# Performance work log

Hardware: AMD Instinct MI355X
Metric: run time of the kernel (lower is better)

## Reference

```python
import jax, jax.numpy as jnp
import numpy as np

B, S, D = 64, 2048, 64

def setup_inputs() -> dict:
    key = jax.random.key(0)
    kq, kk, kv = jax.random.split(key, 3)
    queries = jax.random.normal(kq, (B, S, D), dtype=jnp.float32)
    keys = jax.random.normal(kk, (B, S, D), dtype=jnp.float32)
    values = jax.random.normal(kv, (B, S, D), dtype=jnp.float32)
    return {"queries": queries, "keys": keys, "values": values}

def reference(queries, keys, values):
    # scores: [B, Sq, Sk] = Q @ K^T / sqrt(d)
    d = queries.shape[-1]
    scale = 1.0 / jnp.sqrt(jnp.asarray(d, dtype=queries.dtype))
    scores = jnp.einsum('bqd,bkd->bqk', queries, keys) * scale
    attn = jax.nn.softmax(scores, axis=-1)
    # dropout is identity in eval/reference mode
    return jnp.einsum('bqk,bkd->bqd', attn, values)
```

## Files before the change

kernel.cpp:

```cpp
#include <hip/hip_runtime.h>


typedef short bf16x8 __attribute__((ext_vector_type(8)));
typedef float f32x16 __attribute__((ext_vector_type(16)));

#define SQK 0.18033688011112042f

__device__ __forceinline__ short f2bf(float x) {
  unsigned u = __float_as_uint(x);
  u = (u + 0x7fffu + ((u >> 16) & 1u)) >> 16;
  return (short)u;
}

__device__ __forceinline__ unsigned pk2(float lo, float hi) {
  unsigned r;
  asm("v_cvt_pk_bf16_f32 %0, %1, %2" : "=v"(r) : "v"(lo), "v"(hi));
  return r;
}

#define SM_HALF(ZV, OFF, RS, PUV)                                        \
  {                                                                      \
    float e0 = __builtin_amdgcn_exp2f(ZV[OFF + 0]);                      \
    float e1 = __builtin_amdgcn_exp2f(ZV[OFF + 1]);                      \
    float e2 = __builtin_amdgcn_exp2f(ZV[OFF + 2]);                      \
    float e3 = __builtin_amdgcn_exp2f(ZV[OFF + 3]);                      \
    float e4 = __builtin_amdgcn_exp2f(ZV[OFF + 4]);                      \
    float e5 = __builtin_amdgcn_exp2f(ZV[OFF + 5]);                      \
    float e6 = __builtin_amdgcn_exp2f(ZV[OFF + 6]);                      \
    float e7 = __builtin_amdgcn_exp2f(ZV[OFF + 7]);                      \
    RS += ((e0 + e1) + (e2 + e3)) + ((e4 + e5) + (e6 + e7));             \
    union { bf16x8 v; unsigned u[4]; } pu_;                              \
    pu_.u[0] = pk2(e0, e1); pu_.u[1] = pk2(e2, e3);                      \
    pu_.u[2] = pk2(e4, e5); pu_.u[3] = pk2(e6, e7);                      \
    PUV = pu_.v;                                                         \
  }

__global__ __launch_bounds__(512, 2) void DotProductAttention_44573170598739_kernel(
    const float* __restrict__ Q, const float* __restrict__ K,
    const float* __restrict__ V, float* __restrict__ O) {
  constexpr int S = 2048, D = 64;
  const int b   = blockIdx.x;
  const int q0  = blockIdx.y * 512;
  const int tid = threadIdx.x;
  const int w    = tid >> 6;
  const int lane = tid & 63;
  const int hi   = lane >> 5;
  const int r32  = lane & 31;

  __shared__ __align__(16) short ksh[2][32 * 72];
  __shared__ __align__(16) short vsh[2][64 * 40];

  bf16x8 qf0[4], qf1[4];
#pragma unroll
  for (int dd = 0; dd < 4; ++dd) {
    const float* qp = Q + ((size_t)b * S + q0 + w * 64 + r32) * D + dd * 16 + hi * 8;
    float4 x = ((const float4*)qp)[0];
    float4 y = ((const float4*)qp)[1];
    bf16x8 f;
    f[0] = f2bf(x.x * SQK); f[1] = f2bf(x.y * SQK);
    f[2] = f2bf(x.z * SQK); f[3] = f2bf(x.w * SQK);
    f[4] = f2bf(y.x * SQK); f[5] = f2bf(y.y * SQK);
    f[6] = f2bf(y.z * SQK); f[7] = f2bf(y.w * SQK);
    qf0[dd] = f;
  }
#pragma unroll
  for (int dd = 0; dd < 4; ++dd) {
    const float* qp = Q + ((size_t)b * S + q0 + w * 64 + 32 + r32) * D + dd * 16 + hi * 8;
    float4 x = ((const float4*)qp)[0];
    float4 y = ((const float4*)qp)[1];
    bf16x8 f;
    f[0] = f2bf(x.x * SQK); f[1] = f2bf(x.y * SQK);
    f[2] = f2bf(x.z * SQK); f[3] = f2bf(x.w * SQK);
    f[4] = f2bf(y.x * SQK); f[5] = f2bf(y.y * SQK);
    f[6] = f2bf(y.z * SQK); f[7] = f2bf(y.w * SQK);
    qf1[dd] = f;
  }

  f32x16 oa00 = {}, oa01 = {}, oa10 = {}, oa11 = {};
  float rs0 = 0.f, rs1 = 0.f;
  const f32x16 z16c = {};

  const float* Kb = K + (size_t)b * S * D;
  const float* Vb = V + (size_t)b * S * D;

  const int vcb = 16 * (w >> 2) + (((w & 1) << 3) | ((w & 2) << 1));

  float4 kx;
  float  vv[4];

  kx = ((const float4*)Kb)[tid];
#pragma unroll
  for (int j = 0; j < 4; ++j)
    vv[j] = Vb[(w * 4 + j) * D + lane];
  {
    int f = 4 * tid;
    int row = f >> 6, col = f & 63;
    uint2 pk = { pk2(kx.x, kx.y), pk2(kx.z, kx.w) };
    *(uint2*)&ksh[0][row * 72 + col] = pk;
  }
  {
    uint2 pv = { pk2(vv[0], vv[1]), pk2(vv[2], vv[3]) };
    *(uint2*)&vsh[0][lane * 40 + vcb] = pv;
  }
  kx = ((const float4*)(Kb + 32 * D))[tid];
#pragma unroll
  for (int j = 0; j < 4; ++j)
    vv[j] = Vb[(32 + w * 4 + j) * D + lane];
  __syncthreads();

  int p = 0;
  for (int kt = 0; kt < S; kt += 32, p ^= 1) {
    if (kt + 32 < S) {
      {
        int f = 4 * tid;
        int row = f >> 6, col = f & 63;
        uint2 pk = { pk2(kx.x, kx.y), pk2(kx.z, kx.w) };
        *(uint2*)&ksh[p ^ 1][row * 72 + col] = pk;
      }
      {
        uint2 pv = { pk2(vv[0], vv[1]), pk2(vv[2], vv[3]) };
        *(uint2*)&vsh[p ^ 1][lane * 40 + vcb] = pv;
      }
      if (kt + 64 < S) {
        const float* Kg2 = Kb + (size_t)(kt + 64) * D;
        const float* Vg2 = Vb + (size_t)(kt + 64) * D;
        kx = ((const float4*)Kg2)[tid];
#pragma unroll
        for (int j = 0; j < 4; ++j)
          vv[j] = Vg2[(w * 4 + j) * D + lane];
      }
    }

    const short* kshp = ksh[p];
    const short* vshp = vsh[p];

    bf16x8 kf[4];
#pragma unroll
    for (int dd = 0; dd < 4; ++dd)
      kf[dd] = *(const bf16x8*)&kshp[r32 * 72 + dd * 16 + hi * 8];

    bf16x8 vf00 = *(const bf16x8*)&vshp[r32 * 40 + hi * 8];
    bf16x8 vf01 = *(const bf16x8*)&vshp[(32 + r32) * 40 + hi * 8];
    bf16x8 vf10 = *(const bf16x8*)&vshp[r32 * 40 + 16 + hi * 8];
    bf16x8 vf11 = *(const bf16x8*)&vshp[(32 + r32) * 40 + 16 + hi * 8];

    {
      __builtin_amdgcn_s_setprio(1);
      f32x16 z = __builtin_amdgcn_mfma_f32_32x32x16_bf16(kf[0], qf0[0], z16c, 0, 0, 0);
      z = __builtin_amdgcn_mfma_f32_32x32x16_bf16(kf[1], qf0[1], z, 0, 0, 0);
      z = __builtin_amdgcn_mfma_f32_32x32x16_bf16(kf[2], qf0[2], z, 0, 0, 0);
      z = __builtin_amdgcn_mfma_f32_32x32x16_bf16(kf[3], qf0[3], z, 0, 0, 0);
      __builtin_amdgcn_s_setprio(0);

      bf16x8 pa;
      SM_HALF(z, 0, rs0, pa);
      __builtin_amdgcn_s_setprio(1);
      oa00 = __builtin_amdgcn_mfma_f32_32x32x16_bf16(pa, vf00, oa00, 0, 0, 0);
      oa01 = __builtin_amdgcn_mfma_f32_32x32x16_bf16(pa, vf01, oa01, 0, 0, 0);
      __builtin_amdgcn_s_setprio(0);
      SM_HALF(z, 8, rs0, pa);
      __builtin_amdgcn_s_setprio(1);
      oa00 = __builtin_amdgcn_mfma_f32_32x32x16_bf16(pa, vf10, oa00, 0, 0, 0);
      oa01 = __builtin_amdgcn_mfma_f32_32x32x16_bf16(pa, vf11, oa01, 0, 0, 0);
      __builtin_amdgcn_s_setprio(0);
    }

    {
      __builtin_amdgcn_s_setprio(1);
      f32x16 z = __builtin_amdgcn_mfma_f32_32x32x16_bf16(kf[0], qf1[0], z16c, 0, 0, 0);
      z = __builtin_amdgcn_mfma_f32_32x32x16_bf16(kf[1], qf1[1], z, 0, 0, 0);
      z = __builtin_amdgcn_mfma_f32_32x32x16_bf16(kf[2], qf1[2], z, 0, 0, 0);
      z = __builtin_amdgcn_mfma_f32_32x32x16_bf16(kf[3], qf1[3], z, 0, 0, 0);
      __builtin_amdgcn_s_setprio(0);

      bf16x8 pa;
      SM_HALF(z, 0, rs1, pa);
      __builtin_amdgcn_s_setprio(1);
      oa10 = __builtin_amdgcn_mfma_f32_32x32x16_bf16(pa, vf00, oa10, 0, 0, 0);
      oa11 = __builtin_amdgcn_mfma_f32_32x32x16_bf16(pa, vf01, oa11, 0, 0, 0);
      __builtin_amdgcn_s_setprio(0);
      SM_HALF(z, 8, rs1, pa);
      __builtin_amdgcn_s_setprio(1);
      oa10 = __builtin_amdgcn_mfma_f32_32x32x16_bf16(pa, vf10, oa10, 0, 0, 0);
      oa11 = __builtin_amdgcn_mfma_f32_32x32x16_bf16(pa, vf11, oa11, 0, 0, 0);
      __builtin_amdgcn_s_setprio(0);
    }
    __syncthreads();
  }

  {
    float tot = rs0 + __shfl_xor(rs0, 32);
#pragma unroll
    for (int g = 0; g < 16; ++g) {
      int rq = (g & 3) + 8 * (g >> 2) + 4 * hi;
      float inv = 1.0f / __shfl(tot, rq);
      int q = q0 + w * 64 + rq;
      float* op = O + ((size_t)b * S + q) * D + r32;
      op[0]  = oa00[g] * inv;
      op[32] = oa01[g] * inv;
    }
  }
  {
    float tot = rs1 + __shfl_xor(rs1, 32);
#pragma unroll
    for (int g = 0; g < 16; ++g) {
      int rq = (g & 3) + 8 * (g >> 2) + 4 * hi;
      float inv = 1.0f / __shfl(tot, rq);
      int q = q0 + w * 64 + 32 + rq;
      float* op = O + ((size_t)b * S + q) * D + r32;
      op[0]  = oa10[g] * inv;
      op[32] = oa11[g] * inv;
    }
  }
}

extern "C" void kernel_launch(void* const* d_in, const int* in_sizes, int n_in,
                              void* d_out, int out_size, void* d_ws, size_t ws_size,
                              hipStream_t stream) {
  (void)in_sizes; (void)n_in; (void)out_size; (void)d_ws; (void)ws_size;
  const float* Q = (const float*)d_in[0];
  const float* K = (const float*)d_in[1];
  const float* V = (const float*)d_in[2];
  float* O = (float*)d_out;
  dim3 grid(64, 2048 / 512, 1);
  dim3 block(512, 1, 1);
  hipLaunchKernelGGL(DotProductAttention_44573170598739_kernel,
                     grid, block, 0, stream, Q, K, V, O);
}
```

Before: 179.2 us.

## Double key tile to 64 rows and interleave softmax with second QK MFMA chain

Each loop iteration now processes 64 keys instead of 32, split into two 32-key sub-tiles. This halves the number of barriers and prefetch steps. The per-subtile schedule is reordered so the exp/pack of the first query half overlaps the second QK MFMA chain, and the PV MFMAs interleave with the second half's softmax. The cost is larger LDS buffers (V tile padded to 72) and more prefetch registers, which may pressure occupancy at 2 blocks/CU.

```diff
diff --git a/kernel.cpp b/kernel.cpp
--- a/kernel.cpp
+++ b/kernel.cpp
@@ -47,8 +47,8 @@
   const int hi   = lane >> 5;
   const int r32  = lane & 31;
 
-  __shared__ __align__(16) short ksh[2][32 * 72];
-  __shared__ __align__(16) short vsh[2][64 * 40];
+  __shared__ __align__(16) short ksh[2][64 * 72];
+  __shared__ __align__(16) short vsh[2][64 * 72];
 
   bf16x8 qf0[4], qf1[4];
 #pragma unroll
@@ -83,68 +83,80 @@
   const float* Kb = K + (size_t)b * S * D;
   const float* Vb = V + (size_t)b * S * D;
 
-  const int vcb = 16 * (w >> 2) + (((w & 1) << 3) | ((w & 2) << 1));
-
-  float4 kx;
-  float  vv[4];
-
-  kx = ((const float4*)Kb)[tid];
-#pragma unroll
-  for (int j = 0; j < 4; ++j)
-    vv[j] = Vb[(w * 4 + j) * D + lane];
+  const int vcb = 16 * (w >> 1) + 4 * (w & 1);
+
+  float4 kx[2];
+  float  vv[8];
+
+#pragma unroll
+  for (int i = 0; i < 2; ++i)
+    kx[i] = ((const float4*)Kb)[tid + 512 * i];
+#pragma unroll
+  for (int j = 0; j < 8; ++j)
+    vv[j] = Vb[(w * 8 + j) * D + lane];
+#pragma unroll
+  for (int i = 0; i < 2; ++i) {
+    int f = 4 * tid + 2048 * i;
+    int row = f >> 6, col = f & 63;
+    uint2 pk = { pk2(kx[i].x, kx[i].y), pk2(kx[i].z, kx[i].w) };
+    *(uint2*)&ksh[0][row * 72 + col] = pk;
+  }
   {
-    int f = 4 * tid;
-    int row = f >> 6, col = f & 63;
-    uint2 pk = { pk2(kx.x, kx.y), pk2(kx.z, kx.w) };
-    *(uint2*)&ksh[0][row * 72 + col] = pk;
-  }
-  {
-    uint2 pv = { pk2(vv[0], vv[1]), pk2(vv[2], vv[3]) };
-    *(uint2*)&vsh[0][lane * 40 + vcb] = pv;
-  }
-  kx = ((const float4*)(Kb + 32 * D))[tid];
-#pragma unroll
-  for (int j = 0; j < 4; ++j)
-    vv[j] = Vb[(32 + w * 4 + j) * D + lane];
+    uint2 plo = { pk2(vv[0], vv[1]), pk2(vv[2], vv[3]) };
+    uint2 phi = { pk2(vv[4], vv[5]), pk2(vv[6], vv[7]) };
+    *(uint2*)&vsh[0][lane * 72 + vcb]     = plo;
+    *(uint2*)&vsh[0][lane * 72 + vcb + 8] = phi;
+  }
+#pragma unroll
+  for (int i = 0; i < 2; ++i)
+    kx[i] = ((const float4*)(Kb + 64 * D))[tid + 512 * i];
+#pragma unroll
+  for (int j = 0; j < 8; ++j)
+    vv[j] = Vb[(64 + w * 8 + j) * D + lane];
   __syncthreads();
 
   int p = 0;
-  for (int kt = 0; kt < S; kt += 32, p ^= 1) {
-    if (kt + 32 < S) {
-      {
-        int f = 4 * tid;
+  for (int kt = 0; kt < S; kt += 64, p ^= 1) {
+    if (kt + 64 < S) {
+#pragma unroll
+      for (int i = 0; i < 2; ++i) {
+        int f = 4 * tid + 2048 * i;
         int row = f >> 6, col = f & 63;
-        uint2 pk = { pk2(kx.x, kx.y), pk2(kx.z, kx.w) };
+        uint2 pk = { pk2(kx[i].x, kx[i].y), pk2(kx[i].z, kx[i].w) };
         *(uint2*)&ksh[p ^ 1][row * 72 + col] = pk;
       }
       {
-        uint2 pv = { pk2(vv[0], vv[1]), pk2(vv[2], vv[3]) };
-        *(uint2*)&vsh[p ^ 1][lane * 40 + vcb] = pv;
+        uint2 plo = { pk2(vv[0], vv[1]), pk2(vv[2], vv[3]) };
+        uint2 phi = { pk2(vv[4], vv[5]), pk2(vv[6], vv[7]) };
+        *(uint2*)&vsh[p ^ 1][lane * 72 + vcb]     = plo;
+        *(uint2*)&vsh[p ^ 1][lane * 72 + vcb + 8] = phi;
       }
-      if (kt + 64 < S) {
-        const float* Kg2 = Kb + (size_t)(kt + 64) * D;
-        const float* Vg2 = Vb + (size_t)(kt + 64) * D;
-        kx = ((const float4*)Kg2)[tid];
-#pragma unroll
-        for (int j = 0; j < 4; ++j)
-          vv[j] = Vg2[(w * 4 + j) * D + lane];
+      if (kt + 128 < S) {
+        const float* Kg2 = Kb + (size_t)(kt + 128) * D;
+        const float* Vg2 = Vb + (size_t)(kt + 128) * D;
+#pragma unroll
+        for (int i = 0; i < 2; ++i)
+          kx[i] = ((const float4*)Kg2)[tid + 512 * i];
+#pragma unroll
+        for (int j = 0; j < 8; ++j)
+          vv[j] = Vg2[(w * 8 + j) * D + lane];
       }
     }
 
     const short* kshp = ksh[p];
     const short* vshp = vsh[p];
-
-    bf16x8 kf[4];
-#pragma unroll
-    for (int dd = 0; dd < 4; ++dd)
-      kf[dd] = *(const bf16x8*)&kshp[r32 * 72 + dd * 16 + hi * 8];
-
-    bf16x8 vf00 = *(const bf16x8*)&vshp[r32 * 40 + hi * 8];
-    bf16x8 vf01 = *(const bf16x8*)&vshp[(32 + r32) * 40 + hi * 8];
-    bf16x8 vf10 = *(const bf16x8*)&vshp[r32 * 40 + 16 + hi * 8];
-    bf16x8 vf11 = *(const bf16x8*)&vshp[(32 + r32) * 40 + 16 + hi * 8];
-
-    {
+#pragma unroll
+    for (int t = 0; t < 2; ++t) {
+      bf16x8 kf[4];
+#pragma unroll
+      for (int dd = 0; dd < 4; ++dd)
+        kf[dd] = *(const bf16x8*)&kshp[(t * 32 + r32) * 72 + dd * 16 + hi * 8];
+
+      bf16x8 vf00 = *(const bf16x8*)&vshp[r32 * 72 + t * 32 + hi * 8];
+      bf16x8 vf01 = *(const bf16x8*)&vshp[(32 + r32) * 72 + t * 32 + hi * 8];
+      bf16x8 vf10 = *(const bf16x8*)&vshp[r32 * 72 + t * 32 + 16 + hi * 8];
+      bf16x8 vf11 = *(const bf16x8*)&vshp[(32 + r32) * 72 + t * 32 + 16 + hi * 8];
+
       __builtin_amdgcn_s_setprio(1);
       f32x16 z = __builtin_amdgcn_mfma_f32_32x32x16_bf16(kf[0], qf0[0], z16c, 0, 0, 0);
       z = __builtin_amdgcn_mfma_f32_32x32x16_bf16(kf[1], qf0[1], z, 0, 0, 0);
@@ -152,37 +164,34 @@
       z = __builtin_amdgcn_mfma_f32_32x32x16_bf16(kf[3], qf0[3], z, 0, 0, 0);
       __builtin_amdgcn_s_setprio(0);
 
-      bf16x8 pa;
-      SM_HALF(z, 0, rs0, pa);
-      __builtin_amdgcn_s_setprio(1);
-      oa00 = __builtin_amdgcn_mfma_f32_32x32x16_bf16(pa, vf00, oa00, 0, 0, 0);
-      oa01 = __builtin_amdgcn_mfma_f32_32x32x16_bf16(pa, vf01, oa01, 0, 0, 0);
-      __builtin_amdgcn_s_setprio(0);
-      SM_HALF(z, 8, rs0, pa);
-      __builtin_amdgcn_s_setprio(1);
-      oa00 = __builtin_amdgcn_mfma_f32_32x32x16_bf16(pa, vf10, oa00, 0, 0, 0);
-      oa01 = __builtin_amdgcn_mfma_f32_32x32x16_bf16(pa, vf11, oa01, 0, 0, 0);
-      __builtin_amdgcn_s_setprio(0);
-    }
-
-    {
-      __builtin_amdgcn_s_setprio(1);
-      f32x16 z = __builtin_amdgcn_mfma_f32_32x32x16_bf16(kf[0], qf1[0], z16c, 0, 0, 0);
+      bf16x8 pa0a, pa0b;
+      SM_HALF(z, 0, rs0, pa0a);
+      SM_HALF(z, 8, rs0, pa0b);
+
+      __builtin_amdgcn_s_setprio(1);
+      z = __builtin_amdgcn_mfma_f32_32x32x16_bf16(kf[0], qf1[0], z16c, 0, 0, 0);
       z = __builtin_amdgcn_mfma_f32_32x32x16_bf16(kf[1], qf1[1], z, 0, 0, 0);
       z = __builtin_amdgcn_mfma_f32_32x32x16_bf16(kf[2], qf1[2], z, 0, 0, 0);
       z = __builtin_amdgcn_mfma_f32_32x32x16_bf16(kf[3], qf1[3], z, 0, 0, 0);
       __builtin_amdgcn_s_setprio(0);
 
-      bf16x8 pa;
-      SM_HALF(z, 0, rs1, pa);
-      __builtin_amdgcn_s_setprio(1);
-      oa10 = __builtin_amdgcn_mfma_f32_32x32x16_bf16(pa, vf00, oa10, 0, 0, 0);
-      oa11 = __builtin_amdgcn_mfma_f32_32x32x16_bf16(pa, vf01, oa11, 0, 0, 0);
-      __builtin_amdgcn_s_setprio(0);
-      SM_HALF(z, 8, rs1, pa);
-      __builtin_amdgcn_s_setprio(1);
-      oa10 = __builtin_amdgcn_mfma_f32_32x32x16_bf16(pa, vf10, oa10, 0, 0, 0);
-      oa11 = __builtin_amdgcn_mfma_f32_32x32x16_bf16(pa, vf11, oa11, 0, 0, 0);
+      bf16x8 pa1a, pa1b;
+      __builtin_amdgcn_s_setprio(1);
+      oa00 = __builtin_amdgcn_mfma_f32_32x32x16_bf16(pa0a, vf00, oa00, 0, 0, 0);
+      oa01 = __builtin_amdgcn_mfma_f32_32x32x16_bf16(pa0a, vf01, oa01, 0, 0, 0);
+      __builtin_amdgcn_s_setprio(0);
+      SM_HALF(z, 0, rs1, pa1a);
+      __builtin_amdgcn_s_setprio(1);
+      oa00 = __builtin_amdgcn_mfma_f32_32x32x16_bf16(pa0b, vf10, oa00, 0, 0, 0);
+      oa01 = __builtin_amdgcn_mfma_f32_32x32x16_bf16(pa0b, vf11, oa01, 0, 0, 0);
+      __builtin_amdgcn_s_setprio(0);
+      SM_HALF(z, 8, rs1, pa1b);
+
+      __builtin_amdgcn_s_setprio(1);
+      oa10 = __builtin_amdgcn_mfma_f32_32x32x16_bf16(pa1a, vf00, oa10, 0, 0, 0);
+      oa11 = __builtin_amdgcn_mfma_f32_32x32x16_bf16(pa1a, vf01, oa11, 0, 0, 0);
+      oa10 = __builtin_amdgcn_mfma_f32_32x32x16_bf16(pa1b, vf10, oa10, 0, 0, 0);
+      oa11 = __builtin_amdgcn_mfma_f32_32x32x16_bf16(pa1b, vf11, oa11, 0, 0, 0);
       __builtin_amdgcn_s_setprio(0);
     }
     __syncthreads();
```

New measurement: 181.5 us. No clear change (+1.3%).
